# Performance work log

Measured on AMD Instinct MI355X. Metric: run time of the kernel, lower is better.

## Reference

```python
import jax, jax.numpy as jnp
from jax import lax
import numpy as np


def _conv(x, w, b):
    y = lax.conv_general_dilated(x, w, (1, 1), 'VALID', dimension_numbers=('NCHW', 'OIHW', 'NCHW'))
    return y + b[None, :, None, None]


def _prelu(x, a):
    return jnp.where(x > 0, x, a[None, :, None, None] * x)


def _pnet(x, c1w, c1b, p1, c2w, c2b, p2, c3w, c3b, p3, w41, b41, w42, b42):
    x = _prelu(_conv(x, c1w, c1b), p1)
    H, W = x.shape[2], x.shape[3]
    # MaxPool2d(2,2, ceil_mode=True): pad bottom/right with -inf when odd
    x = lax.reduce_window(x, -jnp.inf, lax.max, (1, 1, 2, 2), (1, 1, 2, 2),
                          ((0, 0), (0, 0), (0, H % 2), (0, W % 2)))
    x = _prelu(_conv(x, c2w, c2b), p2)
    x = _prelu(_conv(x, c3w, c3b), p3)
    a = jax.nn.softmax(_conv(x, w41, b41), axis=1)
    b = _conv(x, w42, b42)
    return b, a


def _nms(boxes, scores, imgidx, valid, thr):
    # masked, fixed-size batched NMS (per-image via coordinate offset trick)
    N = boxes.shape[0]
    order = jnp.argsort(-jnp.where(valid, scores, -1e9))
    b = boxes[order] + imgidx[order].astype(boxes.dtype)[:, None] * 1e5
    v = valid[order]
    x1, y1, x2, y2 = b[:, 0], b[:, 1], b[:, 2], b[:, 3]
    area = jnp.maximum(x2 - x1, 0.0) * jnp.maximum(y2 - y1, 0.0)
    ar = jnp.arange(N)

    def body(i, keep):
        iw = jnp.maximum(jnp.minimum(x2[i], x2) - jnp.maximum(x1[i], x1), 0.0)
        ih = jnp.maximum(jnp.minimum(y2[i], y2) - jnp.maximum(y1[i], y1), 0.0)
        inter = iw * ih
        iou = inter / (area[i] + area - inter + 1e-9)
        return keep & ~((iou > thr) & (ar > i) & keep[i])

    keep = lax.fori_loop(0, N, body, v)
    return order, keep


def _detect(images, c1w, c1b, p1, c2w, c2b, p2, c3w, c3b, p3, w41, b41, w42, b42):
    params = (c1w, c1b, p1, c2w, c2b, p2, c3w, c3b, p3, w41, b41, w42, b42)
    x = jnp.transpose(images, (0, 3, 1, 2))  # NHWC -> NCHW
    B, _, H, W = x.shape
    m = 12.0 / 20.0  # 12 / minsize
    scales = []
    ml, si = min(H, W) * m, m
    while ml >= 12:
        scales.append(si)
        si *= 0.709
        ml *= 0.709
    KS, THR0 = 512, 0.6  # fixed per-scale candidate capacity
    all_b, all_i, all_k = [], [], []
    for scale in scales:
        nh, nw = int(H * scale + 1), int(W * scale + 1)
        im = jax.image.resize(x, (B, 3, nh, nw), method='linear')
        im = (im - 127.5) * 0.0078125
        reg, label = _pnet(im, *params)
        probs = label[:, 1]  # [B,h,w]
        b_, h_, w_ = probs.shape
        yy, xx = jnp.meshgrid(jnp.arange(h_), jnp.arange(w_), indexing='ij')
        bbx = jnp.tile(xx.reshape(-1), b_).astype(x.dtype)
        bby = jnp.tile(yy.reshape(-1), b_).astype(x.dtype)
        # stride=2, cellsize=12 grid-cell -> image-space boxes
        q = [jnp.floor((2 * bbx + 1) / scale), jnp.floor((2 * bby + 1) / scale),
             jnp.floor((2 * bbx + 12) / scale), jnp.floor((2 * bby + 12) / scale)]
        score = probs.reshape(-1)
        reg4 = jnp.transpose(reg, (0, 2, 3, 1)).reshape(-1, 4)
        boxes9 = jnp.concatenate([jnp.stack(q + [score], axis=1), reg4], axis=1)  # [N,9]
        imgidx = jnp.repeat(jnp.arange(b_), h_ * w_)
        k = min(KS, boxes9.shape[0])
        vals, idx = lax.top_k(jnp.where(score >= THR0, score, -1e9), k)
        bsel, isel, vsel = boxes9[idx], imgidx[idx], vals > -1e8
        order, keep = _nms(bsel[:, :4], bsel[:, 4], isel, vsel, 0.5)
        all_b.append(bsel[order])
        all_i.append(isel[order])
        all_k.append(keep)
    boxes = jnp.concatenate(all_b, 0)
    iidx = jnp.concatenate(all_i, 0)
    kp = jnp.concatenate(all_k, 0)
    K2 = min(1024, boxes.shape[0])
    vals, idx = lax.top_k(jnp.where(kp, boxes[:, 4], -1e9), K2)
    b2, i2, v2 = boxes[idx], iidx[idx], vals > -1e8
    order, keep = _nms(b2[:, :4], b2[:, 4], i2, v2, 0.7)
    b2 = b2[order]
    regw, regh = b2[:, 2] - b2[:, 0], b2[:, 3] - b2[:, 1]
    out = jnp.stack([b2[:, 0] + b2[:, 5] * regw, b2[:, 1] + b2[:, 6] * regh,
                     b2[:, 2] + b2[:, 7] * regw, b2[:, 3] + b2[:, 8] * regh, b2[:, 4]], axis=1)
    # rerec: square-ify
    hh, ww = out[:, 3] - out[:, 1], out[:, 2] - out[:, 0]
    l = jnp.maximum(hh, ww)
    x1 = out[:, 0] + ww * 0.5 - l * 0.5
    y1 = out[:, 1] + hh * 0.5 - l * 0.5
    out = jnp.stack([x1, y1, x1 + l, y1 + l, out[:, 4]], axis=1)
    return out * keep[:, None].astype(out.dtype)  # invalid/suppressed rows zeroed


def setup_inputs():
    key = jax.random.key(0)
    ks = jax.random.split(key, 16)
    rn = lambda k, s, sc=0.1: jax.random.normal(k, s, dtype=jnp.float32) * sc
    return {
        'images': jax.random.uniform(ks[0], (8, 768, 768, 3), dtype=jnp.float32) * 255.0,
        'c1w': rn(ks[1], (10, 3, 3, 3)), 'c1b': rn(ks[2], (10,)),
        'p1': 0.25 * jnp.ones((10,), jnp.float32),
        'c2w': rn(ks[3], (16, 10, 3, 3)), 'c2b': rn(ks[4], (16,)),
        'p2': 0.25 * jnp.ones((16,), jnp.float32),
        'c3w': rn(ks[5], (32, 16, 3, 3)), 'c3b': rn(ks[6], (32,)),
        'p3': 0.25 * jnp.ones((32,), jnp.float32),
        'w41': rn(ks[7], (2, 32, 1, 1)), 'b41': rn(ks[8], (2,)),
        'w42': rn(ks[9], (4, 32, 1, 1)), 'b42': rn(ks[10], (4,)),
    }


def reference(images, c1w, c1b, p1, c2w, c2b, p2, c3w, c3b, p3, w41, b41, w42, b42):
    return _detect(images, c1w, c1b, p1, c2w, c2b, p2, c3w, c3b, p3, w41, b41, w42, b42)
```

## Files before the change

kernel.cpp:

```cpp
#include <hip/hip_runtime.h>
#include <stdint.h>

typedef unsigned long long u64;
typedef unsigned int u32;

#define TPB 256
#define NJMAX 12
#define NSC 11

__device__ __forceinline__ int findJob(const int* cum, int nj, int v) {
  int j = 0;
  while (j + 1 < nj && v >= cum[j + 1]) ++j;
  return j;
}

struct MkP { int ns; int nw[NSC]; float invs[NSC], ks[NSC];
             int oxB[NSC], T[NSC], wOff[NSC]; };

__global__ void k_mkweights(int* __restrict__ tX0, int* __restrict__ tCNT,
                            float* __restrict__ tWT, float* __restrict__ tW, MkP P) {
  const int s = blockIdx.x;
  const int nw = P.nw[s];
  const float invs = P.invs[s], ks = P.ks[s];
  const int T = P.T[s];
  for (int ox = threadIdx.x; ox < nw; ox += TPB) {
    float sx = ((float)ox + 0.5f) * invs - 0.5f;
    int x0 = (int)ceilf(sx - ks); if (x0 < 0) x0 = 0;
    int x1 = (int)floorf(sx + ks); if (x1 > 767) x1 = 767;
    float wt = 0.f;
    float* wv = tW + P.wOff[s];
    for (int j = x0; j <= x1; ++j) {
      float w = fmaxf(0.f, 1.f - fabsf(sx - (float)j) / ks);
      wt += w;
      wv[(j - x0) * nw + ox] = w;
    }
    for (int k = x1 - x0 + 1; k < T; ++k) wv[k * nw + ox] = 0.f;
    int g = P.oxB[s] + ox;
    tX0[g] = x0; tCNT[g] = x1 - x0 + 1; tWT[g] = wt;
  }
}

struct DscP { int nj; int N[NJMAX]; int hOff[NJMAX], imgOff[NJMAX];
              int oxB[NJMAX], wOff[NJMAX];
              int cumW[NJMAX + 1], cumR[NJMAX + 1]; };

__global__ void k_mkdesc(int* __restrict__ hd, int* __restrict__ vd,
                         int hdcap, int vdcap, DscP P) {
  int gid = blockIdx.x * TPB + threadIdx.x;
  int totW = P.cumW[P.nj], totR = P.cumR[P.nj];
  if (gid < totW) {
    int j = findJob(P.cumW, P.nj, gid);
    int local = gid - P.cumW[j];
    int N = P.N[j];
    int ox = local % N, c = local / N;
    hd[gid]             = P.hOff[j] + c * 768 * N + ox;
    hd[hdcap + gid]     = c * 769;
    hd[2 * hdcap + gid] = N;
    hd[3 * hdcap + gid] = P.oxB[j] + ox;
    hd[4 * hdcap + gid] = P.wOff[j] + ox;
  }
  if (gid < totR) {
    int j = findJob(P.cumR, P.nj, gid);
    int local = gid - P.cumR[j];
    int N = P.N[j];
    int oy = local % N, q = local / N;
    vd[gid]             = P.hOff[j] + q * 768 * N;
    vd[vdcap + gid]     = P.imgOff[j] + (q * N + oy) * N;
    vd[2 * vdcap + gid] = P.oxB[j] + oy;
    vd[3 * vdcap + gid] = P.wOff[j] + oy;
    vd[4 * vdcap + gid] = N;
  }
}

__global__ void k_resizeH_d(const float* __restrict__ img, float* __restrict__ base,
                            const int* __restrict__ tX0, const int* __restrict__ tCNT,
                            const float* __restrict__ tWT, const float* __restrict__ tW,
                            const int* __restrict__ hd, int hdcap, int total) {
  __shared__ float row[3][769];
  const int y = blockIdx.x, b = blockIdx.y;
  const float* src = img + ((long)b * 768 + y) * 768 * 3;
  for (int t = threadIdx.x; t < 2304; t += TPB) {
    int x = t / 3, c = t - 3 * x;
    row[c][x] = src[t];
  }
  __syncthreads();
  const float* rowF = &row[0][0];
  const long yb = (long)y + 2304L * b;
  for (int t = threadIdx.x; t < total; t += TPB) {
    int A = hd[t];
    int R = hd[hdcap + t];
    int N = hd[2 * hdcap + t];
    int g = hd[3 * hdcap + t];
    int W = hd[4 * hdcap + t];
    int x0 = tX0[g], cnt = tCNT[g];
    float wt = tWT[g];
    const float* wv = tW + W;
    const float* rp = rowF + R + x0;
    float acc = 0.f;
    int k = 0;
    for (; k + 3 < cnt; k += 4) {
      float v0 = rp[k],     w0 = wv[(long)k * N];
      float v1 = rp[k + 1], w1 = wv[(long)(k + 1) * N];
      float v2 = rp[k + 2], w2 = wv[(long)(k + 2) * N];
      float v3 = rp[k + 3], w3 = wv[(long)(k + 3) * N];
      acc += v0 * w0; acc += v1 * w1; acc += v2 * w2; acc += v3 * w3;
    }
    for (; k < cnt; ++k) acc += rp[k] * wv[(long)k * N];
    base[(long)A + (long)N * yb] = acc / wt;
  }
}

__global__ void k_resizeV_row(const float* __restrict__ basep, float* __restrict__ img,
                              const int* __restrict__ tX0, const int* __restrict__ tCNT,
                              const float* __restrict__ tWT, const float* __restrict__ tW,
                              const int* __restrict__ vd, int vdcap, int nRows) {
  int row = blockIdx.x * 4 + (threadIdx.x >> 6);
  if (row >= nRows) return;
  int lane = threadIdx.x & 63;
  int S = vd[row];
  int O = vd[vdcap + row];
  int g = vd[2 * vdcap + row];
  int W = vd[3 * vdcap + row];
  int N = vd[4 * vdcap + row];
  int y0 = tX0[g], cnt = tCNT[g];
  float wt = tWT[g];
  const float* wv = tW + W;
  const float* col0 = basep + S + (long)y0 * N;
  for (int ox = lane; ox < N; ox += 64) {
    const float* col = col0 + ox;
    float acc = 0.f;
    int k = 0;
    for (; k + 3 < cnt; k += 4) {
      float v0 = col[(long)k * N],       w0 = wv[(long)k * N];
      float v1 = col[(long)(k + 1) * N], w1 = wv[(long)(k + 1) * N];
      float v2 = col[(long)(k + 2) * N], w2 = wv[(long)(k + 2) * N];
      float v3 = col[(long)(k + 3) * N], w3 = wv[(long)(k + 3) * N];
      acc += v0 * w0; acc += v1 * w1; acc += v2 * w2; acc += v3 * w3;
    }
    for (; k < cnt; ++k) acc += col[(long)k * N] * wv[(long)k * N];
    img[(long)O + ox] = (acc / wt - 127.5f) * 0.0078125f;
  }
}

__device__ __forceinline__ void conv1pool_body(
    const float* in, const float* w, const float* bias, const float* pr,
    float* out, int H, int W, int b, int px, int py) {
  const int h1 = H - 2, w1 = W - 2;
  const int PH = (h1 + 1) >> 1, PW = (w1 + 1) >> 1;
  if (px >= PW || py >= PH) return;
  const int x0 = px * 2, y0 = py * 2;
  float a00[10], a01[10], a10[10], a11[10];
#pragma unroll
  for (int co = 0; co < 10; ++co) { a00[co] = 0.f; a01[co] = 0.f; a10[co] = 0.f; a11[co] = 0.f; }
  const long HW = (long)H * W;
  const float* pp = in + ((long)b * 3 * H + y0) * W + x0;
  for (int ci = 0; ci < 3; ++ci, pp += HW) {
    const float* r = pp;
    float r00 = r[0], r01 = r[1], r02 = r[2], r03 = r[3]; r += W;
    float r10 = r[0], r11 = r[1], r12 = r[2], r13 = r[3]; r += W;
    float r20 = r[0], r21 = r[1], r22 = r[2], r23 = r[3]; r += W;
    float r30 = r[0], r31 = r[1], r32 = r[2], r33 = r[3];
#pragma unroll
    for (int co = 0; co < 10; ++co) {
      const float* wc = w + ((long)co * 3 + ci) * 9;
      float w0 = wc[0], w1_ = wc[1], w2 = wc[2];
      float w3 = wc[3], w4 = wc[4], w5 = wc[5];
      float w6 = wc[6], w7 = wc[7], w8 = wc[8];
      a00[co] += r00 * w0 + r01 * w1_ + r02 * w2;
      a00[co] += r10 * w3 + r11 * w4 + r12 * w5;
      a00[co] += r20 * w6 + r21 * w7 + r22 * w8;
      a01[co] += r01 * w0 + r02 * w1_ + r03 * w2;
      a01[co] += r11 * w3 + r12 * w4 + r13 * w5;
      a01[co] += r21 * w6 + r22 * w7 + r23 * w8;
      a10[co] += r10 * w0 + r11 * w1_ + r12 * w2;
      a10[co] += r20 * w3 + r21 * w4 + r22 * w5;
      a10[co] += r30 * w6 + r31 * w7 + r32 * w8;
      a11[co] += r11 * w0 + r12 * w1_ + r13 * w2;
      a11[co] += r21 * w3 + r22 * w4 + r23 * w5;
      a11[co] += r31 * w6 + r32 * w7 + r33 * w8;
    }
  }
  const bool vx = (x0 + 1 < w1), vy = (y0 + 1 < h1);
#pragma unroll
  for (int co = 0; co < 10; ++co) {
    const float bb = bias[co], al = pr[co];
    float v = a00[co] + bb; v = v > 0.f ? v : al * v;
    float m = v;
    if (vx) { v = a01[co] + bb; v = v > 0.f ? v : al * v; m = fmaxf(m, v); }
    if (vy) { v = a10[co] + bb; v = v > 0.f ? v : al * v; m = fmaxf(m, v); }
    if (vx && vy) { v = a11[co] + bb; v = v > 0.f ? v : al * v; m = fmaxf(m, v); }
    out[(((long)b * 10 + co) * PH + py) * PW + px] = m;
  }
}

struct C1P { int nj; int nh[NJMAX]; int imgOff[NJMAX], poolOff[NJMAX];
             int t1x[NJMAX]; int cumT[NJMAX + 1]; };

__global__ void k_conv1pool_job(const float* __restrict__ imgb, const float* __restrict__ w,
                                const float* __restrict__ bias, const float* __restrict__ pr,
                                float* __restrict__ poolb, C1P P) {
  int j = findJob(P.cumT, P.nj, blockIdx.x);
  int local = blockIdx.x - P.cumT[j];
  int t1x = P.t1x[j];
  int tX = local % t1x, tY = local / t1x;
  conv1pool_body(imgb + P.imgOff[j], w, bias, pr, poolb + P.poolOff[j],
                 P.nh[j], P.nh[j], blockIdx.z,
                 tX * 16 + (threadIdx.x & 15), tY * 16 + (threadIdx.x >> 4));
}

__device__ __forceinline__ void conv3x3c8_body(
    const float* in, const float* w, const float* bias, const float* pr,
    float* out, int Cin, int Cout, int H, int W, int cog, int b, int x0, int y) {
  const int OH = H - 2, OW = W - 2;
  if (y >= OH || x0 >= OW) return;
  float acc[8][4];
#pragma unroll
  for (int k = 0; k < 8; ++k) { acc[k][0] = 0.f; acc[k][1] = 0.f; acc[k][2] = 0.f; acc[k][3] = 0.f; }
  const float* wp = w + (long)cog * Cin * 9;
  const long HW = (long)H * W;
  const float* pp = in + ((long)b * Cin * H + y) * W + x0;
  for (int ci = 0; ci < Cin; ++ci, pp += HW) {
    const float* r = pp;
    float q00 = r[0], q01 = r[1], q02 = r[2], q03 = r[3], q04 = r[4], q05 = r[5]; r += W;
    float q10 = r[0], q11 = r[1], q12 = r[2], q13 = r[3], q14 = r[4], q15 = r[5]; r += W;
    float q20 = r[0], q21 = r[1], q22 = r[2], q23 = r[3], q24 = r[4], q25 = r[5];
#pragma unroll
    for (int k = 0; k < 8; ++k) {
      const float* wc = wp + ((long)k * Cin + ci) * 9;
      float w0 = wc[0], w1 = wc[1], w2 = wc[2];
      float w3 = wc[3], w4 = wc[4], w5 = wc[5];
      float w6 = wc[6], w7 = wc[7], w8 = wc[8];
      acc[k][0] += q00 * w0 + q01 * w1 + q02 * w2;
      acc[k][1] += q01 * w0 + q02 * w1 + q03 * w2;
      acc[k][2] += q02 * w0 + q03 * w1 + q04 * w2;
      acc[k][3] += q03 * w0 + q04 * w1 + q05 * w2;
      acc[k][0] += q10 * w3 + q11 * w4 + q12 * w5;
      acc[k][1] += q11 * w3 + q12 * w4 + q13 * w5;
      acc[k][2] += q12 * w3 + q13 * w4 + q14 * w5;
      acc[k][3] += q13 * w3 + q14 * w4 + q15 * w5;
      acc[k][0] += q20 * w6 + q21 * w7 + q22 * w8;
      acc[k][1] += q21 * w6 + q22 * w7 + q23 * w8;
      acc[k][2] += q22 * w6 + q23 * w7 + q24 * w8;
      acc[k][3] += q23 * w6 + q24 * w7 + q25 * w8;
    }
  }
  const int rem = OW - x0;
#pragma unroll
  for (int k = 0; k < 8; ++k) {
    const int co = cog + k;
    const float bb = bias[co], al = pr[co];
    float* op = out + (((long)b * Cout + co) * OH + y) * OW + x0;
    float v0 = acc[k][0] + bb; v0 = v0 > 0.f ? v0 : al * v0;
    op[0] = v0;
    if (rem > 1) { float v = acc[k][1] + bb; v = v > 0.f ? v : al * v; op[1] = v; }
    if (rem > 2) { float v = acc[k][2] + bb; v = v > 0.f ? v : al * v; op[2] = v; }
    if (rem > 3) { float v = acc[k][3] + bb; v = v > 0.f ? v : al * v; op[3] = v; }
  }
}

struct CvP { int nj; int H[NJMAX]; int inOff[NJMAX], outOff[NJMAX];
             int tx[NJMAX]; int cumT[NJMAX + 1]; };

__global__ void k_conv3x3c8_job(const float* __restrict__ inb, const float* __restrict__ w,
                                const float* __restrict__ bias, const float* __restrict__ pr,
                                float* __restrict__ outb, int Cin, int Cout, CvP P) {
  int j = findJob(P.cumT, P.nj, blockIdx.x);
  int local = blockIdx.x - P.cumT[j];
  int tx0 = P.tx[j];
  int tX = local % tx0, tY = local / tx0;
  conv3x3c8_body(inb + P.inOff[j], w, bias, pr, outb + P.outOff[j], Cin, Cout,
                 P.H[j], P.H[j], blockIdx.y * 8, blockIdx.z,
                 tX * 64 + (threadIdx.x & 15) * 4, tY * 16 + (threadIdx.x >> 4));
}

__device__ __forceinline__ void head_body(const float* x3, const float* w41,
                                          const float* b41, const float* w42,
                                          const float* b42, float* reg, u64* keys,
                                          int plane, long idx) {
  int b = (int)(idx / plane); int rem = (int)(idx % plane);
  const float* p = x3 + (long)b * 32 * plane + rem;
  float l0 = 0.f, l1 = 0.f, r0 = 0.f, r1 = 0.f, r2 = 0.f, r3 = 0.f;
  for (int c = 0; c < 32; ++c) {
    float v = p[(long)c * plane];
    l0 += v * w41[c];      l1 += v * w41[32 + c];
    r0 += v * w42[c];      r1 += v * w42[32 + c];
    r2 += v * w42[64 + c]; r3 += v * w42[96 + c];
  }
  l0 += b41[0]; l1 += b41[1];
  r0 += b42[0]; r1 += b42[1]; r2 += b42[2]; r3 += b42[3];
  float mx = fmaxf(l0, l1);
  float e0 = expf(l0 - mx), e1 = expf(l1 - mx);
  float s = e1 / (e0 + e1);
  reg[idx * 4 + 0] = r0; reg[idx * 4 + 1] = r1;
  reg[idx * 4 + 2] = r2; reg[idx * 4 + 3] = r3;
  u32 ic = 0xFFFFFFFFu - (u32)idx;
  u64 k = (s >= 0.6f) ? ((((u64)__float_as_uint(s)) << 32) | ic) : (u64)ic;
  keys[idx] = k;
}

struct HdP { int nj; int h3[NJMAX]; int c3Off[NJMAX], kOff[NJMAX];
             int cumC[NJMAX + 1]; };

__global__ void k_head_job(const float* __restrict__ c3b, const float* __restrict__ w41,
                           const float* __restrict__ b41, const float* __restrict__ w42,
                           const float* __restrict__ b42, float* __restrict__ regb,
                           u64* __restrict__ keysb, HdP P) {
  int gid = blockIdx.x * TPB + threadIdx.x;
  if (gid >= P.cumC[P.nj]) return;
  int j = findJob(P.cumC, P.nj, gid);
  int idx = gid - P.cumC[j];
  head_body(c3b + P.c3Off[j], w41, b41, w42, b42,
            regb + 4L * P.kOff[j], keysb + P.kOff[j], P.h3[j] * P.h3[j], idx);
}

__device__ __forceinline__ void bitonic2048(u64* s) {
  for (int k = 2; k <= 2048; k <<= 1) {
    for (int j = k >> 1; j > 0; j >>= 1) {
      for (int i = threadIdx.x; i < 2048; i += TPB) {
        int ixj = i ^ j;
        if (ixj > i) {
          u64 a = s[i], b = s[ixj];
          bool desc = ((i & k) == 0);
          if (desc ? (a < b) : (a > b)) { s[i] = b; s[ixj] = a; }
        }
      }
      __syncthreads();
    }
  }
}

__global__ void k_topk(const u64* __restrict__ in, int n, u64* __restrict__ out, int K) {
  __shared__ u64 s[2048];
  int base = blockIdx.x * 2048;
  for (int t = threadIdx.x; t < 2048; t += TPB) {
    int gi = base + t;
    s[t] = (gi < n) ? in[gi] : 0ULL;
  }
  __syncthreads();
  bitonic2048(s);
  for (int t = threadIdx.x; t < K; t += TPB)
    out[(long)blockIdx.x * K + t] = s[t];
}

struct TkP { int nj; int srcSel[NJMAX]; int srcOff[NJMAX]; int n[NJMAX];
             int dstOff[NJMAX]; int cumB[NJMAX + 1]; };

__global__ void k_topk_job(u64* __restrict__ A, u64* __restrict__ B, TkP P) {
  __shared__ u64 s[2048];
  int j = findJob(P.cumB, P.nj, blockIdx.x);
  int lb = blockIdx.x - P.cumB[j];
  const u64* src = (P.srcSel[j] ? B : A) + P.srcOff[j];
  u64* dst = (P.srcSel[j] ? A : B) + P.dstOff[j];
  int n = P.n[j];
  int base = lb * 2048;
  for (int t = threadIdx.x; t < 2048; t += TPB) {
    int gi = base + t;
    s[t] = (gi < n) ? src[gi] : 0ULL;
  }
  __syncthreads();
  bitonic2048(s);
  for (int t = threadIdx.x; t < 512; t += TPB)
    dst[(long)lb * 512 + t] = s[t];
}

struct TkFP { int nj; int srcSel[NJMAX]; int srcOff[NJMAX]; int n[NJMAX]; int sIdx[NJMAX]; };

__global__ void k_topk_fin(const u64* __restrict__ A, const u64* __restrict__ B,
                           u64* __restrict__ selk, TkFP P) {
  __shared__ u64 s[2048];
  int j = blockIdx.x;
  const u64* src = (P.srcSel[j] ? B : A) + P.srcOff[j];
  int n = P.n[j];
  for (int t = threadIdx.x; t < 2048; t += TPB)
    s[t] = (t < n) ? src[t] : 0ULL;
  __syncthreads();
  bitonic2048(s);
  for (int t = threadIdx.x; t < 512; t += TPB)
    selk[(long)P.sIdx[j] * 512 + t] = s[t];
}

__device__ __forceinline__ void gather_body(const u64* keys, const float* reg,
                                            float* boxes, int h, int w, float scalef,
                                            int i) {
  float* bx = boxes + (long)i * 12;
  u64 key = keys[i];
  if ((key >> 32) == 0ULL) {
    for (int q = 0; q < 12; ++q) bx[q] = 0.f;
    return;
  }
  u32 cell = 0xFFFFFFFFu - (u32)(key & 0xFFFFFFFFu);
  int x = (int)(cell % (u32)w); u32 t2 = cell / (u32)w;
  int y = (int)(t2 % (u32)h); int b = (int)(t2 / (u32)h);
  float fx = (float)x, fy = (float)y;
  bx[0] = floorf((2.f * fx + 1.f) / scalef);
  bx[1] = floorf((2.f * fy + 1.f) / scalef);
  bx[2] = floorf((2.f * fx + 12.f) / scalef);
  bx[3] = floorf((2.f * fy + 12.f) / scalef);
  bx[4] = __uint_as_float((u32)(key >> 32));
  bx[5] = reg[(long)cell * 4 + 0];
  bx[6] = reg[(long)cell * 4 + 1];
  bx[7] = reg[(long)cell * 4 + 2];
  bx[8] = reg[(long)cell * 4 + 3];
  bx[9] = (float)b;
  bx[10] = 1.f;
  bx[11] = 0.f;
}

struct GtP { int nj; int h3[NJMAX]; float scalef[NJMAX]; int kOff[NJMAX]; int sIdx[NJMAX]; };

__global__ void k_gather_job(const u64* __restrict__ selk, const float* __restrict__ regb,
                             float* __restrict__ boxes, GtP P) {
  int j = blockIdx.x >> 1;
  int i = ((blockIdx.x & 1) << 8) + threadIdx.x;
  gather_body(selk + (long)P.sIdx[j] * 512, regb + 4L * P.kOff[j],
              boxes + (long)P.sIdx[j] * 512 * 12, P.h3[j], P.h3[j], P.scalef[j], i);
}

__global__ void k_nms(float* __restrict__ boxes, int per, float thr) {
  __shared__ float sx1[1024], sy1[1024], sx2[1024], sy2[1024], sar[1024];
  __shared__ unsigned char kp[1024];
  __shared__ int snv;
  float* bs = boxes + (long)blockIdx.x * per * 12;
  int N = per;
  if (threadIdx.x == 0) snv = 0;
  __syncthreads();
  for (int i = threadIdx.x; i < N; i += blockDim.x) {
    const float* b = bs + (long)i * 12;
    float off = b[9] * 100000.0f;
    float a0 = b[0] + off, a1 = b[1] + off, a2 = b[2] + off, a3 = b[3] + off;
    sx1[i] = a0; sy1[i] = a1; sx2[i] = a2; sy2[i] = a3;
    sar[i] = fmaxf(a2 - a0, 0.f) * fmaxf(a3 - a1, 0.f);
    bool v = (b[10] != 0.f);
    kp[i] = v;
    if (v) atomicMax(&snv, i + 1);
  }
  __syncthreads();
  int nv = snv;
  for (int i = 0; i < nv; ++i) {
    if (kp[i]) {
      float xi1 = sx1[i], yi1 = sy1[i], xi2 = sx2[i], yi2 = sy2[i], ai = sar[i];
      for (int j = threadIdx.x; j < nv; j += blockDim.x) {
        if (j > i && kp[j]) {
          float iw = fmaxf(fminf(xi2, sx2[j]) - fmaxf(xi1, sx1[j]), 0.f);
          float ih = fmaxf(fminf(yi2, sy2[j]) - fmaxf(yi1, sy1[j]), 0.f);
          float inter = iw * ih;
          float iou = inter / (ai + sar[j] - inter + 1e-9f);
          if (iou > thr) kp[j] = 0;
        }
      }
    }
    __syncthreads();
  }
  for (int i = threadIdx.x; i < N; i += blockDim.x)
    bs[(long)i * 12 + 11] = kp[i] ? 1.f : 0.f;
}

__global__ void k_finalkeys(const float* __restrict__ boxes, u64* __restrict__ keys,
                            int total, int padded) {
  int i = blockIdx.x * blockDim.x + threadIdx.x;
  if (i >= padded) return;
  u64 k = 0ULL;
  if (i < total) {
    const float* b = boxes + (long)i * 12;
    u32 ic = 0xFFFFFFFFu - (u32)i;
    k = (b[11] != 0.f) ? ((((u64)__float_as_uint(b[4])) << 32) | ic) : (u64)ic;
  }
  keys[i] = k;
}

__global__ void k_gatherfinal(const u64* __restrict__ keys, const float* __restrict__ boxes,
                              float* __restrict__ sel) {
  int i = blockIdx.x * blockDim.x + threadIdx.x;
  if (i >= 1024) return;
  u64 key = keys[i];
  float* o = sel + (long)i * 12;
  if ((key >> 32) == 0ULL) {
    for (int q = 0; q < 12; ++q) o[q] = 0.f;
    return;
  }
  u32 bi = 0xFFFFFFFFu - (u32)(key & 0xFFFFFFFFu);
  const float* b = boxes + (long)bi * 12;
  for (int q = 0; q < 12; ++q) o[q] = b[q];
  o[10] = 1.f;
  o[11] = 0.f;
}

__global__ void k_refine(const float* __restrict__ sel, float* __restrict__ out, int N) {
  int i = blockIdx.x * blockDim.x + threadIdx.x;
  if (i >= N) return;
  const float* b = sel + (long)i * 12;
  float keep = b[11];
  float x1 = b[0], y1 = b[1], x2 = b[2], y2 = b[3], sc = b[4];
  float rw = x2 - x1, rh = y2 - y1;
  float o0 = x1 + b[5] * rw;
  float o1 = y1 + b[6] * rh;
  float o2 = x2 + b[7] * rw;
  float o3 = y2 + b[8] * rh;
  float hh = o3 - o1, ww = o2 - o0;
  float l = fmaxf(hh, ww);
  float nx1 = o0 + ww * 0.5f - l * 0.5f;
  float ny1 = o1 + hh * 0.5f - l * 0.5f;
  out[(long)i * 5 + 0] = nx1 * keep;
  out[(long)i * 5 + 1] = ny1 * keep;
  out[(long)i * 5 + 2] = (nx1 + l) * keep;
  out[(long)i * 5 + 3] = (ny1 + l) * keep;
  out[(long)i * 5 + 4] = sc * keep;
}

extern "C" void kernel_launch(void* const* d_in, const int* in_sizes, int n_in,
                              void* d_out, int out_size, void* d_ws, size_t ws_size,
                              hipStream_t stream) {
  (void)in_sizes; (void)n_in; (void)out_size;
  const float* images = (const float*)d_in[0];
  const float* c1w = (const float*)d_in[1];
  const float* c1b = (const float*)d_in[2];
  const float* p1  = (const float*)d_in[3];
  const float* c2w = (const float*)d_in[4];
  const float* c2b = (const float*)d_in[5];
  const float* p2  = (const float*)d_in[6];
  const float* c3w = (const float*)d_in[7];
  const float* c3b = (const float*)d_in[8];
  const float* p3  = (const float*)d_in[9];
  const float* w41 = (const float*)d_in[10];
  const float* b41 = (const float*)d_in[11];
  const float* w42 = (const float*)d_in[12];
  const float* b42 = (const float*)d_in[13];
  float* ws = (float*)d_ws;

  double scl[16]; int nsc = 0;
  {
    double m = 12.0 / 20.0;
    double ml = 768.0 * m;
    double si = m;
    while (ml >= 12.0) { scl[nsc++] = si; si *= 0.709; ml *= 0.709; }
  }

  auto cdiv = [](long a, long b) { return (int)((a + b - 1) / b); };

  int NH[NSC], PH_[NSC], H2[NSC], H3[NSC], OXB[NSC], TT[NSC], WOFF[NSC];
  float INV[NSC], KSF[NSC];
  {
    int oxb = 0, woff = 0;
    for (int s = 0; s < nsc; ++s) {
      int nh = (int)(768.0 * scl[s] + 1.0);
      NH[s] = nh;
      PH_[s] = ((nh - 2) + 1) / 2;
      H2[s] = PH_[s] - 2;
      H3[s] = H2[s] - 2;
      double inv = 1.0 / (((double)nh) / 768.0);
      INV[s] = (float)inv;
      KSF[s] = (float)(inv > 1.0 ? inv : 1.0);
      TT[s] = (int)(2.0f * KSF[s]) + 2;
      OXB[s] = oxb; oxb += nh;
      WOFF[s] = woff; woff += nh * TT[s];
    }
  }

  static const int GA[11] = {0, 1, 2, 3, 4, 5, 6, 7, 8, 9, 10};
  static const int G1[7] = {0, 5, 6, 7, 8, 9, 10};
  static const int G2[4] = {1, 2, 3, 4};

  struct Layout {
    long HT, IMG, POOL, C2, REG, KEYS, SCR, SEL, BOX, FK, FS, SF, TBL, HD, VD, extent;
    int hdcap, vdcap;
  };

  auto calcLayout = [&](const int* const* gps, const int* gn, int ng,
                        int hdcap, int vdcap, Layout& L) {
    long htA = 0, c3A = 0, imgA = 0, poolA = 0, c2A = 0, cellsA = 0, scrA = 0;
    for (int g = 0; g < ng; ++g) {
      long ht = 0, c3 = 0, im = 0, pl = 0, c2s = 0, ck = 0, sc = 0;
      for (int q = 0; q < gn[g]; ++q) {
        int s = gps[g][q];
        ht += 24L * 768 * NH[s];
        im += 24L * NH[s] * NH[s];
        pl += 80L * PH_[s] * PH_[s];
        c2s += 128L * H2[s] * H2[s];
        c3 += 256L * H3[s] * H3[s];
        long cells = 8L * H3[s] * H3[s];
        ck += cells;
        sc += 512L * ((cells + 2047) / 2048);
      }
      if (ht > htA) htA = ht; if (c3 > c3A) c3A = c3; if (im > imgA) imgA = im;
      if (pl > poolA) poolA = pl; if (c2s > c2A) c2A = c2s;
      if (ck > cellsA) cellsA = ck; if (sc > scrA) scrA = sc;
    }
    long htR = htA > c3A ? htA : c3A;
    auto al = [](long v) { return (v + 15) & ~15L; };
    long off = 0;
    L.HT = off;   off += al(htR);
    L.IMG = off;  off += al(imgA);
    L.POOL = off; off += al(poolA);
    L.C2 = off;   off += al(c2A);
    L.REG = off;  off += al(4 * cellsA);
    L.KEYS = off; off += al(2 * cellsA);
    L.SCR = off;  off += al(2 * scrA + 16384);
    L.SEL = off;  off += al(11264);
    L.BOX = off;  off += al(67584);
    L.FK = off;   off += al(16384);
    L.FS = off;   off += al(2048);
    L.SF = off;   off += al(12288);
    L.TBL = off;  off += al(12288 + 24000);
    L.HD = off;   off += al((long)ng * 5 * hdcap);
    L.VD = off;   off += al((long)ng * 5 * vdcap);
    L.extent = off;
    L.hdcap = hdcap; L.vdcap = vdcap;
  };

  Layout LA, LB;
  {
    const int* gpsA[1] = {GA}; int gnA[1] = {11};
    calcLayout(gpsA, gnA, 1, 8192, 56320, LA);
    const int* gpsB[2] = {G1, G2}; int gnB[2] = {7, 4};
    calcLayout(gpsB, gnB, 2, 2560, 20480, LB);
  }
  bool big = (ws_size >= (size_t)LA.extent * 4);
  const Layout& L = big ? LA : LB;
  const int* GS[2]; int GN[2]; int ngroups;
  if (big) { GS[0] = GA; GN[0] = 11; ngroups = 1; }
  else { GS[0] = G1; GN[0] = 7; GS[1] = G2; GN[1] = 4; ngroups = 2; }

  u64* keys  = (u64*)(ws + L.KEYS);
  u64* scr   = (u64*)(ws + L.SCR);
  u64* selk  = (u64*)(ws + L.SEL);
  u64* fkeys = (u64*)(ws + L.FK);
  u64* fsel  = (u64*)(ws + L.FS);
  float* boxes = ws + L.BOX;
  float* self  = ws + L.SF;
  int*   tX0  = (int*)(ws + L.TBL);
  int*   tCNT = (int*)(ws + L.TBL + 4096);
  float* tWT  = ws + L.TBL + 8192;
  float* tW   = ws + L.TBL + 12288;

  {
    MkP P; P.ns = nsc;
    for (int s = 0; s < nsc; ++s) {
      P.nw[s] = NH[s]; P.invs[s] = INV[s]; P.ks[s] = KSF[s];
      P.oxB[s] = OXB[s]; P.T[s] = TT[s]; P.wOff[s] = WOFF[s];
    }
    k_mkweights<<<nsc, TPB, 0, stream>>>(tX0, tCNT, tWT, tW, P);
  }

  int imgOff[2][NJMAX], poolOff[2][NJMAX], c2Off[2][NJMAX], c3Off[2][NJMAX],
      htOff[2][NJMAX], kOff[2][NJMAX], cells[2][NJMAX];
  int cumWtot[2], cumRtot[2];
  for (int g = 0; g < ngroups; ++g) {
    long ch = 0, ci = 0, cp = 0, c2 = 0, c3 = 0, ck = 0;
    int cw = 0, cr = 0;
    for (int q = 0; q < GN[g]; ++q) {
      int s = GS[g][q];
      htOff[g][q] = (int)ch;  ch += 24L * 768 * NH[s];
      imgOff[g][q] = (int)ci; ci += 24L * NH[s] * NH[s];
      poolOff[g][q] = (int)cp; cp += 80L * PH_[s] * PH_[s];
      c2Off[g][q] = (int)c2;  c2 += 128L * H2[s] * H2[s];
      c3Off[g][q] = (int)c3;  c3 += 256L * H3[s] * H3[s];
      kOff[g][q] = (int)ck;   cells[g][q] = 8 * H3[s] * H3[s]; ck += cells[g][q];
      cw += 3 * NH[s]; cr += 24 * NH[s];
    }
    cumWtot[g] = cw; cumRtot[g] = cr;
  }

  for (int g = 0; g < ngroups; ++g) {
    DscP P; P.nj = GN[g];
    int cw = 0, cr = 0;
    for (int q = 0; q < GN[g]; ++q) {
      int s = GS[g][q];
      P.N[q] = NH[s]; P.hOff[q] = htOff[g][q]; P.imgOff[q] = imgOff[g][q];
      P.oxB[q] = OXB[s]; P.wOff[q] = WOFF[s];
      P.cumW[q] = cw; cw += 3 * NH[s];
      P.cumR[q] = cr; cr += 24 * NH[s];
    }
    P.cumW[GN[g]] = cw; P.cumR[GN[g]] = cr;
    int* hd = (int*)(ws + L.HD) + (long)g * 5 * L.hdcap;
    int* vd = (int*)(ws + L.VD) + (long)g * 5 * L.vdcap;
    int tot = cw > cr ? cw : cr;
    k_mkdesc<<<cdiv(tot, TPB), TPB, 0, stream>>>(hd, vd, L.hdcap, L.vdcap, P);
  }

  for (int g = 0; g < ngroups; ++g) {
    const int* gs = GS[g];
    int nj = GN[g];
    int* hd = (int*)(ws + L.HD) + (long)g * 5 * L.hdcap;
    int* vd = (int*)(ws + L.VD) + (long)g * 5 * L.vdcap;
    {
      dim3 gh(768, 8, 1);
      k_resizeH_d<<<gh, TPB, 0, stream>>>(images, ws + L.HT, tX0, tCNT, tWT, tW,
                                          hd, L.hdcap, cumWtot[g]);
    }
    k_resizeV_row<<<cdiv(cumRtot[g], 4), TPB, 0, stream>>>(
        ws + L.HT, ws + L.IMG, tX0, tCNT, tWT, tW, vd, L.vdcap, cumRtot[g]);
    {
      C1P P; P.nj = nj; int ct = 0;
      for (int q = 0; q < nj; ++q) {
        int s = gs[q];
        P.nh[q] = NH[s];
        P.imgOff[q] = imgOff[g][q]; P.poolOff[q] = poolOff[g][q];
        int t1x = cdiv(PH_[s], 16);
        P.t1x[q] = t1x;
        P.cumT[q] = ct; ct += t1x * t1x;
      }
      P.cumT[nj] = ct;
      dim3 gg(ct, 1, 8);
      k_conv1pool_job<<<gg, TPB, 0, stream>>>(ws + L.IMG, c1w, c1b, p1, ws + L.POOL, P);
    }
    {
      CvP P; P.nj = nj; int ct = 0;
      for (int q = 0; q < nj; ++q) {
        int s = gs[q];
        P.H[q] = PH_[s];
        P.inOff[q] = poolOff[g][q]; P.outOff[q] = c2Off[g][q];
        int tx = cdiv(H2[s], 64), ty = cdiv(H2[s], 16);
        P.tx[q] = tx;
        P.cumT[q] = ct; ct += tx * ty;
      }
      P.cumT[nj] = ct;
      dim3 gg(ct, 2, 8);
      k_conv3x3c8_job<<<gg, TPB, 0, stream>>>(ws + L.POOL, c2w, c2b, p2, ws + L.C2,
                                              10, 16, P);
    }
    {
      CvP P; P.nj = nj; int ct = 0;
      for (int q = 0; q < nj; ++q) {
        int s = gs[q];
        P.H[q] = H2[s];
        P.inOff[q] = c2Off[g][q]; P.outOff[q] = c3Off[g][q];
        int tx = cdiv(H3[s], 64), ty = cdiv(H3[s], 16);
        P.tx[q] = tx;
        P.cumT[q] = ct; ct += tx * ty;
      }
      P.cumT[nj] = ct;
      dim3 gg(ct, 4, 8);
      k_conv3x3c8_job<<<gg, TPB, 0, stream>>>(ws + L.C2, c3w, c3b, p3, ws + L.HT,
                                              16, 32, P);
    }
    {
      HdP P; P.nj = nj; int cc = 0;
      for (int q = 0; q < nj; ++q) {
        int s = gs[q];
        P.h3[q] = H3[s];
        P.c3Off[q] = c3Off[g][q]; P.kOff[q] = kOff[g][q];
        P.cumC[q] = cc; cc += cells[g][q];
      }
      P.cumC[nj] = cc;
      k_head_job<<<cdiv(cc, TPB), TPB, 0, stream>>>(ws + L.HT, w41, b41, w42, b42,
                                                    ws + L.REG, keys, P);
    }
    {
      int bOff[NJMAX];
      {
        int c = 0;
        for (int q = 0; q < nj; ++q) { bOff[q] = c; c += 512 * cdiv(cells[g][q], 2048); }
      }
      long nCur[NJMAX]; int par[NJMAX];
      for (int q = 0; q < nj; ++q) { nCur[q] = cells[g][q]; par[q] = 0; }
      while (true) {
        TkP P; P.nj = 0; int cum = 0; int act[NJMAX];
        for (int q = 0; q < nj; ++q) {
          if (nCur[q] > 2048) {
            int r = P.nj++;
            act[r] = q;
            int blocks = cdiv(nCur[q], 2048);
            P.srcSel[r] = par[q];
            P.srcOff[r] = par[q] ? bOff[q] : kOff[g][q];
            P.dstOff[r] = par[q] ? kOff[g][q] : bOff[q];
            P.n[r] = (int)nCur[q];
            P.cumB[r] = cum; cum += blocks;
          }
        }
        P.cumB[P.nj] = cum;
        if (P.nj == 0) break;
        k_topk_job<<<cum, TPB, 0, stream>>>(keys, scr, P);
        for (int r = 0; r < P.nj; ++r) {
          int q = act[r];
          nCur[q] = 512L * cdiv(nCur[q], 2048);
          par[q] ^= 1;
        }
      }
      TkFP F; F.nj = nj;
      for (int q = 0; q < nj; ++q) {
        F.srcSel[q] = par[q];
        F.srcOff[q] = par[q] ? bOff[q] : kOff[g][q];
        F.n[q] = (int)nCur[q];
        F.sIdx[q] = gs[q];
      }
      k_topk_fin<<<nj, TPB, 0, stream>>>(keys, scr, selk, F);
    }
    {
      GtP P; P.nj = nj;
      for (int q = 0; q < nj; ++q) {
        int s = gs[q];
        P.h3[q] = H3[s]; P.scalef[q] = (float)scl[s]; P.kOff[q] = kOff[g][q];
        P.sIdx[q] = s;
      }
      k_gather_job<<<2 * nj, TPB, 0, stream>>>(selk, ws + L.REG, boxes, P);
    }
  }

  k_nms<<<nsc, TPB, 0, stream>>>(boxes, 512, 0.5f);

  int total = nsc * 512;
  k_finalkeys<<<cdiv(8192, TPB), TPB, 0, stream>>>(boxes, fkeys, total, 8192);
  k_topk<<<4, TPB, 0, stream>>>(fkeys, 8192, scr, 1024);
  k_topk<<<2, TPB, 0, stream>>>(scr, 4096, keys, 1024);
  k_topk<<<1, TPB, 0, stream>>>(keys, 2048, fsel, 1024);
  k_gatherfinal<<<4, TPB, 0, stream>>>(fsel, boxes, self);
  k_nms<<<1, TPB, 0, stream>>>(self, 1024, 0.7f);
  k_refine<<<4, TPB, 0, stream>>>(self, (float*)d_out, 1024);
}
```

Measured before the change: 1.114 ms.

## Block NMS into 64-box chunks resolved in-wavefront with shuffles

Restructures the greedy NMS loop so that each chunk of 64 boxes is resolved by a single wavefront using lane shuffles, and only then are later boxes suppressed against the chunk's survivors in parallel. This replaces one block-wide barrier per candidate with one per 64-box chunk, cutting the serial synchronisation cost. In exchange the other waves sit idle during the intra-chunk pass, and the per-thread suppression loop does more shared-memory reads.

```diff
diff --git a/kernel.cpp b/kernel.cpp
--- a/kernel.cpp
+++ b/kernel.cpp
@@ -419,6 +419,7 @@
 __global__ void k_nms(float* __restrict__ boxes, int per, float thr) {
   __shared__ float sx1[1024], sy1[1024], sx2[1024], sy2[1024], sar[1024];
   __shared__ unsigned char kp[1024];
+  __shared__ unsigned char kb[64];
   __shared__ int snv;
   float* bs = boxes + (long)blockIdx.x * per * 12;
   int N = per;
@@ -436,18 +437,45 @@
   }
   __syncthreads();
   int nv = snv;
-  for (int i = 0; i < nv; ++i) {
-    if (kp[i]) {
-      float xi1 = sx1[i], yi1 = sy1[i], xi2 = sx2[i], yi2 = sy2[i], ai = sar[i];
-      for (int j = threadIdx.x; j < nv; j += blockDim.x) {
-        if (j > i && kp[j]) {
-          float iw = fmaxf(fminf(xi2, sx2[j]) - fmaxf(xi1, sx1[j]), 0.f);
-          float ih = fmaxf(fminf(yi2, sy2[j]) - fmaxf(yi1, sy1[j]), 0.f);
+  const int wave = threadIdx.x >> 6, lane = threadIdx.x & 63;
+  for (int base = 0; base < nv; base += 64) {
+    const int lim = (nv - base < 64) ? (nv - base) : 64;
+    if (wave == 0) {
+      int gi = base + lane;
+      bool ok = (lane < lim) && kp[gi];
+      float bx1 = 0.f, by1 = 0.f, bx2 = 0.f, by2 = 0.f, ba = 0.f;
+      if (lane < lim) { bx1 = sx1[gi]; by1 = sy1[gi]; bx2 = sx2[gi]; by2 = sy2[gi]; ba = sar[gi]; }
+      for (int i = 0; i < lim; ++i) {
+        int ki = __shfl((int)ok, i);
+        float xi1 = __shfl(bx1, i), yi1 = __shfl(by1, i);
+        float xi2 = __shfl(bx2, i), yi2 = __shfl(by2, i);
+        float ai = __shfl(ba, i);
+        if (ki && lane > i && ok) {
+          float iw = fmaxf(fminf(xi2, bx2) - fmaxf(xi1, bx1), 0.f);
+          float ih = fmaxf(fminf(yi2, by2) - fmaxf(yi1, by1), 0.f);
           float inter = iw * ih;
-          float iou = inter / (ai + sar[j] - inter + 1e-9f);
-          if (iou > thr) kp[j] = 0;
+          float iou = inter / (ai + ba - inter + 1e-9f);
+          if (iou > thr) ok = false;
         }
       }
+      if (lane < lim) kp[gi] = ok ? 1 : 0;
+      kb[lane] = (lane < lim && ok) ? 1 : 0;
+    }
+    __syncthreads();
+    for (int j = base + 64 + threadIdx.x; j < nv; j += blockDim.x) {
+      if (!kp[j]) continue;
+      float jx2 = sx2[j], jy2 = sy2[j], jx1 = sx1[j], jy1 = sy1[j], ja = sar[j];
+      bool ok = true;
+      for (int i = 0; i < lim && ok; ++i) {
+        if (!kb[i]) continue;
+        int gi = base + i;
+        float iw = fmaxf(fminf(sx2[gi], jx2) - fmaxf(sx1[gi], jx1), 0.f);
+        float ih = fmaxf(fminf(sy2[gi], jy2) - fmaxf(sy1[gi], jy1), 0.f);
+        float inter = iw * ih;
+        float iou = inter / (sar[gi] + ja - inter + 1e-9f);
+        if (iou > thr) ok = false;
+      }
+      if (!ok) kp[j] = 0;
     }
     __syncthreads();
   }
```

New measurement: 1.114 ms. No clear change (-0.0%).
